# Performance work log

Measured on AMD Instinct MI355X. Metric: run time of the kernel, lower is better.

Reference implementation:

```python
import jax, jax.numpy as jnp
import numpy as np

EPS = 1e-6
GAMMA_INIT = 1e-5


def setup_inputs() -> dict:
    key = jax.random.key(0)
    N, D = 32768, 2048
    x = jax.random.normal(key, (N, D), dtype=jnp.float32)
    weight = jnp.ones((D,), dtype=jnp.float32)
    gamma = jnp.full((D,), GAMMA_INIT, dtype=jnp.float32)
    return {"x": x, "weight": weight, "gamma": gamma, "k": 256}


def reference(x, weight, gamma, k):
    # RMSNorm (computed in float32, cast back to input dtype)
    xf = x.astype(jnp.float32)
    rms = jax.lax.rsqrt(jnp.mean(xf * xf, axis=-1, keepdims=True) + EPS)
    x_norm = (xf * rms).astype(x.dtype) * weight  # [N, D]

    # Top-k magnitude thresholding per row
    mags = jnp.abs(x_norm)
    topk_vals, _ = jax.lax.top_k(mags, k)          # [N, k]
    threshold = topk_vals[:, -1:]                  # [N, 1] k-th largest magnitude
    mask = (mags >= threshold).astype(x_norm.dtype)

    # LayerScale + residual
    return x + (x_norm * mask) * gamma
```

## Files before the change

### kernel.cpp

```cpp
#include <hip/hip_runtime.h>
#include <cstddef>

#define THREADS 256
#define DDIM 2048
#define NBINS 2048

__global__ __launch_bounds__(THREADS) void sparse_topk_rmsnorm_kernel(
    const float* __restrict__ x,
    const float* __restrict__ weight,
    const float* __restrict__ gamma,
    const int* __restrict__ kp,
    float* __restrict__ out)
{
    const int tid  = threadIdx.x;
    const int lane = tid & 63;
    const int wid  = tid >> 6;
    const long row = blockIdx.x;

    __shared__ unsigned hist[NBINS];
    __shared__ float    wsumf[4];
    __shared__ unsigned wtot[4];
    __shared__ unsigned s_prefix;
    __shared__ unsigned s_kk;

    const float4* x4 = (const float4*)(x + row * (long)DDIM);
    const float4* w4 = (const float4*)weight;
    const float4* g4 = (const float4*)gamma;

    float4 a  = x4[tid];
    float4 b  = x4[tid + 256];
    float4 wa = w4[tid];
    float4 wb = w4[tid + 256];
    float4 ga = g4[tid];
    float4 gb = g4[tid + 256];

    const uint4 zero4 = make_uint4(0u, 0u, 0u, 0u);
    uint4* h4 = (uint4*)hist;
    h4[2*tid]     = zero4;
    h4[2*tid + 1] = zero4;

    float ss = a.x*a.x + a.y*a.y + a.z*a.z + a.w*a.w
             + b.x*b.x + b.y*b.y + b.z*b.z + b.w*b.w;
    #pragma unroll
    for (int off = 32; off > 0; off >>= 1)
        ss += __shfl_down(ss, off, 64);
    if (lane == 0) wsumf[wid] = ss;
    __syncthreads();
    const float total = wsumf[0] + wsumf[1] + wsumf[2] + wsumf[3];
    const float rms = rsqrtf(total * (1.0f / (float)DDIM) + 1e-6f);

    float nx[8];
    unsigned mb[8];
    nx[0] = a.x * rms * wa.x;  nx[1] = a.y * rms * wa.y;
    nx[2] = a.z * rms * wa.z;  nx[3] = a.w * rms * wa.w;
    nx[4] = b.x * rms * wb.x;  nx[5] = b.y * rms * wb.y;
    nx[6] = b.z * rms * wb.z;  nx[7] = b.w * rms * wb.w;
    #pragma unroll
    for (int i = 0; i < 8; ++i)
        mb[i] = __float_as_uint(fabsf(nx[i]));

    unsigned kk = (unsigned)kp[0];
    unsigned prefix = 0;

    const int      shifts[3] = {20, 9, 0};
    const unsigned dmask[3]  = {0x7FFu, 0x7FFu, 0x1FFu};
    const unsigned himask[3] = {0u, 0xFFF00000u, 0xFFFFFE00u};

    #pragma unroll
    for (int r = 0; r < 3; ++r) {
        const int shift = shifts[r];
        #pragma unroll
        for (int i = 0; i < 8; ++i) {
            if ((mb[i] & himask[r]) == prefix)
                atomicAdd(&hist[(mb[i] >> shift) & dmask[r]], 1u);
        }
        __syncthreads();

        uint4 h0 = h4[2*tid];
        uint4 h1 = h4[2*tid + 1];
        unsigned c[8] = {h0.x, h0.y, h0.z, h0.w, h1.x, h1.y, h1.z, h1.w};
        unsigned sfx[8];
        sfx[7] = c[7];
        #pragma unroll
        for (int i = 6; i >= 0; --i) sfx[i] = sfx[i+1] + c[i];
        const unsigned T = sfx[0];
        unsigned suf = T;
        #pragma unroll
        for (int off = 1; off < 64; off <<= 1) {
            unsigned t = __shfl_down(suf, off, 64);
            if (lane + off < 64) suf += t;
        }
        if (lane == 0) wtot[wid] = suf;
        __syncthreads();

        unsigned above = suf - T;
        #pragma unroll
        for (int w = 0; w < 4; ++w)
            if (w > wid) above += wtot[w];
        #pragma unroll
        for (int i = 0; i < 8; ++i) {
            const unsigned cge = above + sfx[i];
            const unsigned cgt = cge - c[i];
            if (cgt < kk && kk <= cge) {
                s_prefix = prefix | ((unsigned)(8*tid + i) << shift);
                s_kk = kk - cgt;
            }
        }
        if (r < 2) {
            h4[2*tid]     = zero4;
            h4[2*tid + 1] = zero4;
        }
        __syncthreads();
        prefix = s_prefix;
        kk = s_kk;
    }

    const unsigned thr = prefix;

    float4 o1, o2;
    o1.x = a.x + (mb[0] >= thr ? nx[0] * ga.x : 0.0f);
    o1.y = a.y + (mb[1] >= thr ? nx[1] * ga.y : 0.0f);
    o1.z = a.z + (mb[2] >= thr ? nx[2] * ga.z : 0.0f);
    o1.w = a.w + (mb[3] >= thr ? nx[3] * ga.w : 0.0f);
    o2.x = b.x + (mb[4] >= thr ? nx[4] * gb.x : 0.0f);
    o2.y = b.y + (mb[5] >= thr ? nx[5] * gb.y : 0.0f);
    o2.z = b.z + (mb[6] >= thr ? nx[6] * gb.z : 0.0f);
    o2.w = b.w + (mb[7] >= thr ? nx[7] * gb.w : 0.0f);

    float4* out4 = (float4*)(out + row * (long)DDIM);
    out4[tid]       = o1;
    out4[tid + 256] = o2;
}

extern "C" void kernel_launch(void* const* d_in, const int* in_sizes, int n_in,
                              void* d_out, int out_size, void* d_ws, size_t ws_size,
                              hipStream_t stream) {
    const float* x      = (const float*)d_in[0];
    const float* weight = (const float*)d_in[1];
    const float* gamma  = (const float*)d_in[2];
    const int*   kp     = (const int*)d_in[3];
    const int D = in_sizes[1];
    const int N = in_sizes[0] / D;
    (void)n_in; (void)out_size; (void)d_ws; (void)ws_size;

    sparse_topk_rmsnorm_kernel<<<dim3(N), dim3(THREADS), 0, stream>>>(
        x, weight, gamma, kp, (float*)d_out);
}
```

Measured before the change: 455.6 us.

## Prefilter radix select with Gaussian-estimated pivot and early exit, nontemporal IO

Estimates a lower-bound pivot for the k-th magnitude from the row's weighted variance using an inverse-Gaussian tail approximation. Elements below the pivot are skipped in the histogram atomics, and the loop falls back to pivot zero if too few elements pass. Radix rounds exit early when the target bin holds one element or exactly the remainder, resolving the threshold with a shared atomicMax or atomicMin. x loads and output stores become nontemporal. The aim is fewer LDS atomics and fewer radix passes, at the cost of extra reductions and transcendentals, a dynamic loop, and an estimate that only pays off for roughly Gaussian inputs.

```diff
diff --git a/kernel.cpp b/kernel.cpp
--- a/kernel.cpp
+++ b/kernel.cpp
@@ -4,6 +4,8 @@
 #define THREADS 256
 #define DDIM 2048
 #define NBINS 2048
+
+typedef float f4 __attribute__((ext_vector_type(4)));
 
 __global__ __launch_bounds__(THREADS) void sparse_topk_rmsnorm_kernel(
     const float* __restrict__ x,
@@ -17,18 +19,21 @@
     const int wid  = tid >> 6;
     const long row = blockIdx.x;
 
-    __shared__ unsigned hist[NBINS];
+    __shared__ __align__(16) unsigned hist[NBINS];
     __shared__ float    wsumf[4];
+    __shared__ float    wsumw[4];
     __shared__ unsigned wtot[4];
     __shared__ unsigned s_prefix;
     __shared__ unsigned s_kk;
+    __shared__ unsigned s_cnt;
+    __shared__ unsigned s_thr;
 
-    const float4* x4 = (const float4*)(x + row * (long)DDIM);
+    const f4*     x4 = (const f4*)(x + row * (long)DDIM);
     const float4* w4 = (const float4*)weight;
     const float4* g4 = (const float4*)gamma;
 
-    float4 a  = x4[tid];
-    float4 b  = x4[tid + 256];
+    f4 a = __builtin_nontemporal_load(x4 + tid);
+    f4 b = __builtin_nontemporal_load(x4 + tid + 256);
     float4 wa = w4[tid];
     float4 wb = w4[tid + 256];
     float4 ga = g4[tid];
@@ -39,15 +44,24 @@
     h4[2*tid]     = zero4;
     h4[2*tid + 1] = zero4;
 
+    float xw[8];
+    xw[0]=a.x*wa.x; xw[1]=a.y*wa.y; xw[2]=a.z*wa.z; xw[3]=a.w*wa.w;
+    xw[4]=b.x*wb.x; xw[5]=b.y*wb.y; xw[6]=b.z*wb.z; xw[7]=b.w*wb.w;
     float ss = a.x*a.x + a.y*a.y + a.z*a.z + a.w*a.w
              + b.x*b.x + b.y*b.y + b.z*b.z + b.w*b.w;
+    float ssw = xw[0]*xw[0]+xw[1]*xw[1]+xw[2]*xw[2]+xw[3]*xw[3]
+              + xw[4]*xw[4]+xw[5]*xw[5]+xw[6]*xw[6]+xw[7]*xw[7];
     #pragma unroll
-    for (int off = 32; off > 0; off >>= 1)
-        ss += __shfl_down(ss, off, 64);
-    if (lane == 0) wsumf[wid] = ss;
+    for (int off = 32; off > 0; off >>= 1) {
+        ss  += __shfl_down(ss,  off, 64);
+        ssw += __shfl_down(ssw, off, 64);
+    }
+    if (lane == 0) { wsumf[wid] = ss; wsumw[wid] = ssw; }
     __syncthreads();
     const float total = wsumf[0] + wsumf[1] + wsumf[2] + wsumf[3];
-    const float rms = rsqrtf(total * (1.0f / (float)DDIM) + 1e-6f);
+    const float totw  = wsumw[0] + wsumw[1] + wsumw[2] + wsumw[3];
+    const float rms   = rsqrtf(total * (1.0f / (float)DDIM) + 1e-6f);
+    const float sigma = rms * sqrtf(fmaxf(totw, 0.0f) * (1.0f / (float)DDIM));
 
     float nx[8];
     unsigned mb[8];
@@ -59,25 +73,36 @@
     for (int i = 0; i < 8; ++i)
         mb[i] = __float_as_uint(fabsf(nx[i]));
 
-    unsigned kk = (unsigned)kp[0];
-    unsigned prefix = 0;
+    int k0 = kp[0];
+    if (k0 < 1)    k0 = 1;
+    if (k0 > DDIM) k0 = DDIM;
+    unsigned kk = (unsigned)k0;
 
-    const int      shifts[3] = {20, 9, 0};
-    const unsigned dmask[3]  = {0x7FFu, 0x7FFu, 0x1FFu};
-    const unsigned himask[3] = {0u, 0xFFF00000u, 0xFFFFFE00u};
+    const float f2 = (float)kk * (0.5f / (float)DDIM);
+    float z = sqrtf(fmaxf(-2.0f * __logf(f2), 0.0f));
+    z = sqrtf(fmaxf(-2.0f * __logf(f2 * 2.5066283f * z), 0.0f));
+    z = sqrtf(fmaxf(-2.0f * __logf(f2 * 2.5066283f * z), 0.0f));
+    const float piv = 0.75f * z * sigma;
+    unsigned pv = (piv > 0.0f && piv < 3.0e38f) ? __float_as_uint(piv) : 0u;
 
-    #pragma unroll
-    for (int r = 0; r < 3; ++r) {
-        const int shift = shifts[r];
+    unsigned prefix = 0u, thr = 0u;
+    int r = 0;
+    for (;;) {
+        const int      shift  = (r == 0) ? 20 : (r == 1) ? 9 : 0;
+        const unsigned dmask  = (r == 2) ? 0x1FFu : 0x7FFu;
+        const unsigned himask = (r == 0) ? 0u
+                              : (r == 1) ? 0xFFF00000u : 0xFFFFFE00u;
+
         #pragma unroll
         for (int i = 0; i < 8; ++i) {
-            if ((mb[i] & himask[r]) == prefix)
-                atomicAdd(&hist[(mb[i] >> shift) & dmask[r]], 1u);
+            const unsigned m = mb[i];
+            if (m >= pv && (m & himask) == prefix)
+                atomicAdd(&hist[(m >> shift) & dmask], 1u);
         }
         __syncthreads();
 
-        uint4 h0 = h4[2*tid];
-        uint4 h1 = h4[2*tid + 1];
+        const uint4 h0 = h4[2*tid];
+        const uint4 h1 = h4[2*tid + 1];
         unsigned c[8] = {h0.x, h0.y, h0.z, h0.w, h1.x, h1.y, h1.z, h1.w};
         unsigned sfx[8];
         sfx[7] = c[7];
@@ -87,7 +112,7 @@
         unsigned suf = T;
         #pragma unroll
         for (int off = 1; off < 64; off <<= 1) {
-            unsigned t = __shfl_down(suf, off, 64);
+            const unsigned t = __shfl_down(suf, off, 64);
             if (lane + off < 64) suf += t;
         }
         if (lane == 0) wtot[wid] = suf;
@@ -102,22 +127,47 @@
             const unsigned cge = above + sfx[i];
             const unsigned cgt = cge - c[i];
             if (cgt < kk && kk <= cge) {
+                const unsigned kloc = kk - cgt;
                 s_prefix = prefix | ((unsigned)(8*tid + i) << shift);
-                s_kk = kk - cgt;
+                s_kk  = kloc;
+                s_cnt = c[i];
+                s_thr = (kloc == 1u) ? 0u : 0xFFFFFFFFu;
             }
         }
+        if (tid == 0 && (above + sfx[0]) < kk) s_cnt = 0u;
         if (r < 2) {
             h4[2*tid]     = zero4;
             h4[2*tid + 1] = zero4;
         }
         __syncthreads();
+
+        const unsigned cnt = s_cnt;
+        if (cnt == 0u) { pv = 0u; continue; }
         prefix = s_prefix;
-        kk = s_kk;
+        const unsigned kloc = s_kk;
+        if (r == 2) { thr = prefix; break; }
+        if (kloc == 1u || kloc == cnt) {
+            const unsigned hm = (r == 0) ? 0xFFF00000u : 0xFFFFFE00u;
+            if (kloc == 1u) {
+                #pragma unroll
+                for (int i = 0; i < 8; ++i)
+                    if (mb[i] >= pv && (mb[i] & hm) == prefix)
+                        atomicMax(&s_thr, mb[i]);
+            } else {
+                #pragma unroll
+                for (int i = 0; i < 8; ++i)
+                    if (mb[i] >= pv && (mb[i] & hm) == prefix)
+                        atomicMin(&s_thr, mb[i]);
+            }
+            __syncthreads();
+            thr = s_thr;
+            break;
+        }
+        kk = kloc;
+        ++r;
     }
 
-    const unsigned thr = prefix;
-
-    float4 o1, o2;
+    f4 o1, o2;
     o1.x = a.x + (mb[0] >= thr ? nx[0] * ga.x : 0.0f);
     o1.y = a.y + (mb[1] >= thr ? nx[1] * ga.y : 0.0f);
     o1.z = a.z + (mb[2] >= thr ? nx[2] * ga.z : 0.0f);
@@ -127,9 +177,9 @@
     o2.z = b.z + (mb[6] >= thr ? nx[6] * gb.z : 0.0f);
     o2.w = b.w + (mb[7] >= thr ? nx[7] * gb.w : 0.0f);
 
-    float4* out4 = (float4*)(out + row * (long)DDIM);
-    out4[tid]       = o1;
-    out4[tid + 256] = o2;
+    f4* o4 = (f4*)(out + row * (long)DDIM);
+    __builtin_nontemporal_store(o1, o4 + tid);
+    __builtin_nontemporal_store(o2, o4 + tid + 256);
 }
 
 extern "C" void kernel_launch(void* const* d_in, const int* in_sizes, int n_in,
```

Measured after the change: 451.2 us. Within noise of the previous version (-0.9%).
